# Kernel optimization log

Hardware: AMD Instinct MI355X
Metric: run time of the kernel (lower is better)

## Reference

```python
import jax, jax.numpy as jnp
import numpy as np

N = 16384

def _gcn_norm(edge_index, n):
    # PyG GCNConv: add self-loops, symmetric normalization D^-1/2 A_hat D^-1/2
    src = jnp.concatenate([edge_index[0], jnp.arange(n)])
    dst = jnp.concatenate([edge_index[1], jnp.arange(n)])
    deg = jax.ops.segment_sum(jnp.ones(src.shape[0], jnp.float32), dst, num_segments=n)
    dinv = jnp.where(deg > 0, jax.lax.rsqrt(deg), 0.0)
    w = dinv[src] * dinv[dst]  # [E + N]
    return src, dst, w

def _gcn_conv(x, W, b, src, dst, w, n):
    h = x @ W                                   # transform then propagate
    msg = w[:, None] * h[src]                   # gather + scale
    out = jax.ops.segment_sum(msg, dst, num_segments=n)  # scatter-add at targets
    return out + b

def setup_inputs() -> dict:
    key = jax.random.key(0)
    ks = jax.random.split(key, 8)
    E = 262144
    x = jax.random.normal(ks[0], (N, 128), jnp.float32)
    edge_index = jax.random.randint(ks[1], (2, E), 0, N, dtype=jnp.int64)
    W1 = jax.random.normal(ks[2], (128, 64), jnp.float32) * 0.1
    b1 = jnp.zeros((64,), jnp.float32)
    Wmu = jax.random.normal(ks[3], (64, 32), jnp.float32) * 0.1
    bmu = jnp.zeros((32,), jnp.float32)
    Wls = jax.random.normal(ks[4], (64, 32), jnp.float32) * 0.1
    bls = jnp.zeros((32,), jnp.float32)
    eps = jax.random.normal(ks[5], (N, 32), jnp.float32)
    return {"x": x, "edge_index": edge_index, "W1": W1, "b1": b1,
            "Wmu": Wmu, "bmu": bmu, "Wls": Wls, "bls": bls, "eps": eps}

def reference(x, edge_index, W1, b1, Wmu, bmu, Wls, bls, eps):
    n = x.shape[0]
    src, dst, w = _gcn_norm(edge_index, n)
    h = jax.nn.relu(_gcn_conv(x, W1, b1, src, dst, w, n))
    mu = _gcn_conv(h, Wmu, bmu, src, dst, w, n)
    logstd = _gcn_conv(h, Wls, bls, src, dst, w, n)
    z = mu + eps * jnp.exp(logstd)              # reparameterize
    adj_recon = jax.nn.sigmoid(z @ z.T)         # dense inner-product decode [N,N]
    return adj_recon, mu, logstd
```

## Files before the change

### kernel.cpp

```cpp
#include <hip/hip_runtime.h>

#define NN 16384
#define FIN 128
#define FH 64
#define FO 32

typedef __attribute__((ext_vector_type(8))) short bf16x8;
typedef __attribute__((ext_vector_type(4))) float f32x4;

__device__ inline unsigned short f2bf(float f) {
    unsigned int u = __float_as_uint(f);
    unsigned int r = (u + 0x7FFFu + ((u >> 16) & 1u)) >> 16;
    return (unsigned short)r;
}
__device__ inline float bf2f(unsigned short b) {
    return __uint_as_float((unsigned int)b << 16);
}


__global__ void k_zero(int* __restrict__ cnt) {
    int i = blockIdx.x * 256 + threadIdx.x;
    cnt[i] = 0;
}

__global__ void k_count(const int* __restrict__ dst, int* __restrict__ cnt, int E) {
    int e = blockIdx.x * 256 + threadIdx.x;
    if (e < E) atomicAdd(&cnt[dst[e] & (NN - 1)], 1);
}

__global__ __launch_bounds__(256) void k_scan(const int* __restrict__ cnt,
                                              int* __restrict__ row) {
    __shared__ int part[256];
    __shared__ int off[257];
    int t = threadIdx.x;
    int base = t * 64;
    int s = 0;
    for (int i = 0; i < 64; ++i) s += cnt[base + i];
    part[t] = s;
    __syncthreads();
    if (t == 0) {
        int a = 0;
        for (int i = 0; i < 256; ++i) { off[i] = a; a += part[i]; }
        off[256] = a;
    }
    __syncthreads();
    int a = off[t];
    for (int i = 0; i < 64; ++i) { row[base + i] = a; a += cnt[base + i]; }
    if (t == 0) row[NN] = off[256];
}

__global__ void k_dinv(const int* __restrict__ cnt, float* __restrict__ dinv,
                       int* __restrict__ cur) {
    int i = blockIdx.x * 256 + threadIdx.x;
    dinv[i] = rsqrtf((float)cnt[i] + 1.0f);
    cur[i] = 0;
}

__global__ void k_fill(const int* __restrict__ src, const int* __restrict__ dst,
                       const int* __restrict__ row, int* __restrict__ cur,
                       const float* __restrict__ dinv,
                       int* __restrict__ csr_s, float* __restrict__ csr_w, int E) {
    int e = blockIdx.x * 256 + threadIdx.x;
    if (e >= E) return;
    int s = src[e] & (NN - 1), d = dst[e] & (NN - 1);
    int pos = atomicAdd(&cur[d], 1);
    int slot = row[d] + pos;
    csr_s[slot] = s;
    csr_w[slot] = dinv[s] * dinv[d];
}


__global__ void k_h0(const float* __restrict__ x, const float* __restrict__ W1,
                     float* __restrict__ h0) {
    int row = blockIdx.x * 4 + (threadIdx.x >> 6);
    int col = threadIdx.x & 63;
    const float* xr = x + row * FIN;
    float acc = 0.f;
#pragma unroll 8
    for (int k = 0; k < FIN; ++k)
        acc = fmaf(xr[k], W1[k * FH + col], acc);
    h0[row * FH + col] = acc;
}

__global__ void k_t(const float* __restrict__ h, const float* __restrict__ Wmu,
                    const float* __restrict__ Wls, float* __restrict__ tmu,
                    float* __restrict__ tls) {
    int row = blockIdx.x * 4 + (threadIdx.x >> 6);
    int l = threadIdx.x & 63;
    const float* hr = h + row * FH;
    const float* W = (l < 32) ? Wmu : Wls;
    int c = l & 31;
    float acc = 0.f;
#pragma unroll 8
    for (int k = 0; k < FH; ++k)
        acc = fmaf(hr[k], W[k * FO + c], acc);
    if (l < 32) tmu[row * FO + c] = acc;
    else        tls[row * FO + c] = acc;
}


__global__ void k_prop1g(const int* __restrict__ row, const int* __restrict__ csr_s,
                         const float* __restrict__ csr_w, const float* __restrict__ dinv,
                         const float* __restrict__ h0, const float* __restrict__ b1,
                         float* __restrict__ h) {
    int t = blockIdx.x * 256 + threadIdx.x;
    int i = t >> 6, l = t & 63;
    int beg = row[i], end = row[i + 1];
    float di = dinv[i];
    float acc = di * di * h0[i * FH + l];
    for (int j = beg; j < end; ++j) {
        int s = csr_s[j];
        float w = csr_w[j];
        acc = fmaf(w, h0[s * FH + l], acc);
    }
    float v = acc + b1[l];
    h[i * FH + l] = v > 0.f ? v : 0.f;
}

__global__ void k_prop2g(const int* __restrict__ row, const int* __restrict__ csr_s,
                         const float* __restrict__ csr_w, const float* __restrict__ dinv,
                         const float* __restrict__ tmu, const float* __restrict__ tls,
                         const float* __restrict__ bmu, const float* __restrict__ bls,
                         const float* __restrict__ eps,
                         float* __restrict__ mu_out, float* __restrict__ ls_out,
                         unsigned short* __restrict__ zh, unsigned short* __restrict__ zl) {
    int t = blockIdx.x * 256 + threadIdx.x;
    int i = t >> 6, l = t & 63;
    int c = l & 31;
    int beg = row[i], end = row[i + 1];
    const float* tp = (l < 32) ? tmu : tls;
    float di = dinv[i];
    float acc = di * di * tp[i * FO + c];
    for (int j = beg; j < end; ++j) {
        int s = csr_s[j];
        float w = csr_w[j];
        acc = fmaf(w, tp[s * FO + c], acc);
    }
    float v = acc + ((l < 32) ? bmu[c] : bls[c]);
    if (l < 32) mu_out[i * FO + c] = v;
    else        ls_out[i * FO + c] = v;
    float other = __shfl_xor(v, 32);
    if (l < 32) {
        float zf = fmaf(eps[i * FO + c], __expf(other), v);
        unsigned short hb = f2bf(zf);
        zh[i * FO + c] = hb;
        zl[i * FO + c] = f2bf(zf - bf2f(hb));
    }
}

__global__ __launch_bounds__(256) void k_decode(const unsigned short* __restrict__ zh,
                                                const unsigned short* __restrict__ zl,
                                                float* __restrict__ out) {
    __shared__ float slab[4][16][264];
    int bj = blockIdx.x & 15, bi = blockIdx.x >> 4;
    int w = threadIdx.x >> 6;
    int l = threadIdx.x & 63;
    int lr = l & 15, lg = l >> 4;

    auto ld = [&](const unsigned short* p, int t) -> bf16x8 {
        return *(const bf16x8*)(p + ((size_t)t * 16 + lr) * FO + lg * 8);
    };

    bf16x8 rh = ld(zh, bi), rl = ld(zl, bi);

    int ctbase = bj * 64 + w * 16;
    bf16x8 ch[16], cl[16];
#pragma unroll
    for (int j = 0; j < 16; ++j) {
        ch[j] = ld(zh, ctbase + j);
        cl[j] = ld(zl, ctbase + j);
    }

#pragma unroll
    for (int j = 0; j < 16; ++j) {
        f32x4 a = {0.f, 0.f, 0.f, 0.f};
        a = __builtin_amdgcn_mfma_f32_16x16x32_bf16(ch[j], rh, a, 0, 0, 0);
        a = __builtin_amdgcn_mfma_f32_16x16x32_bf16(ch[j], rl, a, 0, 0, 0);
        a = __builtin_amdgcn_mfma_f32_16x16x32_bf16(cl[j], rh, a, 0, 0, 0);
        float4 v;
        v.x = __builtin_amdgcn_rcpf(1.f + __expf(-a[0]));
        v.y = __builtin_amdgcn_rcpf(1.f + __expf(-a[1]));
        v.z = __builtin_amdgcn_rcpf(1.f + __expf(-a[2]));
        v.w = __builtin_amdgcn_rcpf(1.f + __expf(-a[3]));
        *(float4*)&slab[w][lr][j * 16 + lg * 4] = v;
    }

#pragma unroll
    for (int r = 0; r < 16; ++r) {
        f32x4 v = *(const f32x4*)&slab[w][r][l * 4];
        f32x4* dst = (f32x4*)(out + ((size_t)(bi * 16 + r)) * NN
                              + bj * 1024 + w * 256 + l * 4);
        __builtin_nontemporal_store(v, dst);
    }
}


extern "C" void kernel_launch(void* const* d_in, const int* in_sizes, int n_in,
                              void* d_out, int out_size, void* d_ws, size_t ws_size,
                              hipStream_t stream) {
    const float* x    = (const float*)d_in[0];
    const int*   ei   = (const int*)d_in[1];
    const float* W1   = (const float*)d_in[2];
    const float* b1   = (const float*)d_in[3];
    const float* Wmu  = (const float*)d_in[4];
    const float* bmu  = (const float*)d_in[5];
    const float* Wls  = (const float*)d_in[6];
    const float* bls  = (const float*)d_in[7];
    const float* eps  = (const float*)d_in[8];

    int E = in_sizes[1] / 2;
    const int* src = ei;
    const int* dst = ei + E;

    float* ws = (float*)d_ws;
    float* dinv  = ws;
    int*   cnt   = (int*)(dinv + NN);
    int*   row   = cnt + NN;
    int*   cur   = row + NN + 16;
    int*   csr_s = cur + NN;
    float* csr_w = (float*)(csr_s + E);
    float* h0    = csr_w + E;
    float* h     = h0 + (size_t)NN * FH;
    float* tmu   = h  + (size_t)NN * FH;
    float* tls   = tmu + (size_t)NN * FO;
    unsigned short* zh = (unsigned short*)(tls + (size_t)NN * FO);
    unsigned short* zl = zh + (size_t)NN * FO;

    float* adj    = (float*)d_out;
    float* mu_out = adj + (size_t)NN * NN;
    float* ls_out = mu_out + (size_t)NN * FO;

    k_zero<<<NN / 256, 256, 0, stream>>>(cnt);
    k_count<<<(E + 255) / 256, 256, 0, stream>>>(dst, cnt, E);
    k_scan<<<1, 256, 0, stream>>>(cnt, row);
    k_dinv<<<NN / 256, 256, 0, stream>>>(cnt, dinv, cur);
    k_fill<<<(E + 255) / 256, 256, 0, stream>>>(src, dst, row, cur, dinv, csr_s, csr_w, E);
    k_h0<<<NN / 4, 256, 0, stream>>>(x, W1, h0);
    k_prop1g<<<NN * FH / 256, 256, 0, stream>>>(row, csr_s, csr_w, dinv, h0, b1, h);
    k_t<<<NN / 4, 256, 0, stream>>>(h, Wmu, Wls, tmu, tls);
    k_prop2g<<<NN * FH / 256, 256, 0, stream>>>(row, csr_s, csr_w, dinv, tmu, tls,
                                                bmu, bls, eps, mu_out, ls_out, zh, zl);
    k_decode<<<(NN / 16) * (NN / 1024), 256, 0, stream>>>(zh, zl, adj);
}
```

Before: 334.9 us.

## Fuse graph preprocessing kernels and restructure decode into two half-tile passes

Folds the dinv/cur initialisation into the scan kernel, merges CSR fill with the x@W1 transform into one launch, and fuses the first propagation with the second-layer weight transform using wave shuffles, removing the intermediate h buffer and several launches. The decode kernel now loads column tiles on the fly in two groups of eight, halving the LDS slab and requesting four blocks per CU for higher occupancy. The decode output is dominated by the 1 GiB adjacency write, so launch savings are small relative to total time, and the on-the-fly loads may expose more latency. There is also a leftover empty loop.

Measured after the change: 311.0 us. 7.1% less time.

```diff
diff --git a/kernel.cpp b/kernel.cpp
--- a/kernel.cpp
+++ b/kernel.cpp
@@ -29,7 +29,9 @@
 }
 
 __global__ __launch_bounds__(256) void k_scan(const int* __restrict__ cnt,
-                                              int* __restrict__ row) {
+                                              int* __restrict__ row,
+                                              float* __restrict__ dinv,
+                                              int* __restrict__ cur) {
     __shared__ int part[256];
     __shared__ int off[257];
     int t = threadIdx.x;
@@ -45,64 +47,47 @@
     }
     __syncthreads();
     int a = off[t];
-    for (int i = 0; i < 64; ++i) { row[base + i] = a; a += cnt[base + i]; }
+    for (int i = 0; i < 64; ++i) {
+        int c = cnt[base + i];
+        row[base + i] = a; a += c;
+        dinv[base + i] = rsqrtf((float)c + 1.0f);
+        cur[base + i] = 0;
+    }
     if (t == 0) row[NN] = off[256];
 }
 
-__global__ void k_dinv(const int* __restrict__ cnt, float* __restrict__ dinv,
-                       int* __restrict__ cur) {
-    int i = blockIdx.x * 256 + threadIdx.x;
-    dinv[i] = rsqrtf((float)cnt[i] + 1.0f);
-    cur[i] = 0;
-}
-
-__global__ void k_fill(const int* __restrict__ src, const int* __restrict__ dst,
-                       const int* __restrict__ row, int* __restrict__ cur,
-                       const float* __restrict__ dinv,
-                       int* __restrict__ csr_s, float* __restrict__ csr_w, int E) {
-    int e = blockIdx.x * 256 + threadIdx.x;
-    if (e >= E) return;
-    int s = src[e] & (NN - 1), d = dst[e] & (NN - 1);
-    int pos = atomicAdd(&cur[d], 1);
-    int slot = row[d] + pos;
-    csr_s[slot] = s;
-    csr_w[slot] = dinv[s] * dinv[d];
-}
-
-
-__global__ void k_h0(const float* __restrict__ x, const float* __restrict__ W1,
-                     float* __restrict__ h0) {
-    int row = blockIdx.x * 4 + (threadIdx.x >> 6);
-    int col = threadIdx.x & 63;
-    const float* xr = x + row * FIN;
-    float acc = 0.f;
+__global__ void k_fill_h0(const int* __restrict__ src, const int* __restrict__ dst,
+                          const int* __restrict__ row, int* __restrict__ cur,
+                          const float* __restrict__ dinv,
+                          int* __restrict__ csr_s, float* __restrict__ csr_w, int E, int nf,
+                          const float* __restrict__ x, const float* __restrict__ W1,
+                          float* __restrict__ h0) {
+    int b = blockIdx.x;
+    if (b < nf) {
+        int e = b * 256 + threadIdx.x;
+        if (e >= E) return;
+        int s = src[e] & (NN - 1), d = dst[e] & (NN - 1);
+        int pos = atomicAdd(&cur[d], 1);
+        int slot = row[d] + pos;
+        csr_s[slot] = s;
+        csr_w[slot] = dinv[s] * dinv[d];
+    } else {
+        int r = (b - nf) * 4 + (threadIdx.x >> 6);
+        int col = threadIdx.x & 63;
+        const float* xr = x + r * FIN;
+        float acc = 0.f;
 #pragma unroll 8
-    for (int k = 0; k < FIN; ++k)
-        acc = fmaf(xr[k], W1[k * FH + col], acc);
-    h0[row * FH + col] = acc;
-}
-
-__global__ void k_t(const float* __restrict__ h, const float* __restrict__ Wmu,
-                    const float* __restrict__ Wls, float* __restrict__ tmu,
-                    float* __restrict__ tls) {
-    int row = blockIdx.x * 4 + (threadIdx.x >> 6);
-    int l = threadIdx.x & 63;
-    const float* hr = h + row * FH;
-    const float* W = (l < 32) ? Wmu : Wls;
-    int c = l & 31;
-    float acc = 0.f;
-#pragma unroll 8
-    for (int k = 0; k < FH; ++k)
-        acc = fmaf(hr[k], W[k * FO + c], acc);
-    if (l < 32) tmu[row * FO + c] = acc;
-    else        tls[row * FO + c] = acc;
-}
-
-
-__global__ void k_prop1g(const int* __restrict__ row, const int* __restrict__ csr_s,
+        for (int k = 0; k < FIN; ++k)
+            acc = fmaf(xr[k], W1[k * FH + col], acc);
+        h0[r * FH + col] = acc;
+    }
+}
+
+__global__ void k_prop1t(const int* __restrict__ row, const int* __restrict__ csr_s,
                          const float* __restrict__ csr_w, const float* __restrict__ dinv,
                          const float* __restrict__ h0, const float* __restrict__ b1,
-                         float* __restrict__ h) {
+                         const float* __restrict__ Wmu, const float* __restrict__ Wls,
+                         float* __restrict__ tmu, float* __restrict__ tls) {
     int t = blockIdx.x * 256 + threadIdx.x;
     int i = t >> 6, l = t & 63;
     int beg = row[i], end = row[i + 1];
@@ -114,7 +99,16 @@
         acc = fmaf(w, h0[s * FH + l], acc);
     }
     float v = acc + b1[l];
-    h[i * FH + l] = v > 0.f ? v : 0.f;
+    v = v > 0.f ? v : 0.f;
+
+    const float* W = (l < 32) ? Wmu : Wls;
+    int c = l & 31;
+    float o = 0.f;
+#pragma unroll
+    for (int k = 0; k < FH; ++k)
+        o = fmaf(__shfl(v, k), W[k * FO + c], o);
+    if (l < 32) tmu[i * FO + c] = o;
+    else        tls[i * FO + c] = o;
 }
 
 __global__ void k_prop2g(const int* __restrict__ row, const int* __restrict__ csr_s,
@@ -148,10 +142,10 @@
     }
 }
 
-__global__ __launch_bounds__(256) void k_decode(const unsigned short* __restrict__ zh,
-                                                const unsigned short* __restrict__ zl,
-                                                float* __restrict__ out) {
-    __shared__ float slab[4][16][264];
+__global__ __launch_bounds__(256, 4) void k_decode(const unsigned short* __restrict__ zh,
+                                                   const unsigned short* __restrict__ zl,
+                                                   float* __restrict__ out) {
+    __shared__ float slab[4][16][136];
     int bj = blockIdx.x & 15, bi = blockIdx.x >> 4;
     int w = threadIdx.x >> 6;
     int l = threadIdx.x & 63;
@@ -164,33 +158,39 @@
     bf16x8 rh = ld(zh, bi), rl = ld(zl, bi);
 
     int ctbase = bj * 64 + w * 16;
-    bf16x8 ch[16], cl[16];
-#pragma unroll
-    for (int j = 0; j < 16; ++j) {
-        ch[j] = ld(zh, ctbase + j);
-        cl[j] = ld(zl, ctbase + j);
-    }
-
-#pragma unroll
-    for (int j = 0; j < 16; ++j) {
-        f32x4 a = {0.f, 0.f, 0.f, 0.f};
-        a = __builtin_amdgcn_mfma_f32_16x16x32_bf16(ch[j], rh, a, 0, 0, 0);
-        a = __builtin_amdgcn_mfma_f32_16x16x32_bf16(ch[j], rl, a, 0, 0, 0);
-        a = __builtin_amdgcn_mfma_f32_16x16x32_bf16(cl[j], rh, a, 0, 0, 0);
-        float4 v;
-        v.x = __builtin_amdgcn_rcpf(1.f + __expf(-a[0]));
-        v.y = __builtin_amdgcn_rcpf(1.f + __expf(-a[1]));
-        v.z = __builtin_amdgcn_rcpf(1.f + __expf(-a[2]));
-        v.w = __builtin_amdgcn_rcpf(1.f + __expf(-a[3]));
-        *(float4*)&slab[w][lr][j * 16 + lg * 4] = v;
-    }
-
-#pragma unroll
-    for (int r = 0; r < 16; ++r) {
-        f32x4 v = *(const f32x4*)&slab[w][r][l * 4];
-        f32x4* dst = (f32x4*)(out + ((size_t)(bi * 16 + r)) * NN
-                              + bj * 1024 + w * 256 + l * 4);
-        __builtin_nontemporal_store(v, dst);
+#pragma unroll
+    for (int g = 0; g < 2; ++g) {
+#pragma unroll
+        for (int j = 0; j < 8; ++j) {
+            int ct = ctbase + g * 8 + j;
+            bf16x8 ch = ld(zh, ct);
+            bf16x8 cl = ld(zl, ct);
+            f32x4 a = {0.f, 0.f, 0.f, 0.f};
+            a = __builtin_amdgcn_mfma_f32_16x16x32_bf16(ch, rh, a, 0, 0, 0);
+            a = __builtin_amdgcn_mfma_f32_16x16x32_bf16(ch, rl, a, 0, 0, 0);
+            a = __builtin_amdgcn_mfma_f32_16x16x32_bf16(cl, rh, a, 0, 0, 0);
+            float4 v;
+            v.x = __builtin_amdgcn_rcpf(1.f + __expf(-a[0]));
+            v.y = __builtin_amdgcn_rcpf(1.f + __expf(-a[1]));
+            v.z = __builtin_amdgcn_rcpf(1.f + __expf(-a[2]));
+            v.w = __builtin_amdgcn_rcpf(1.f + __expf(-a[3]));
+            *(float4*)&slab[w][lr][j * 16 + lg * 4] = v;
+        }
+        size_t cbase = (size_t)bj * 1024 + w * 256 + g * 128;
+#pragma unroll
+        for (int inst = 0; inst < 8; ++inst) {
+            int r = inst * 2 + (l >> 5);
+            int f4 = l & 31;
+            f32x4 v = *(const f32x4*)&slab[w][r][f4 * 4];
+            f32x4* dst = (f32x4*)(out + ((size_t)(bi * 16 + r)) * NN + cbase + f4 * 4);
+            __builtin_nontemporal_store(v, dst);
+        }
+#pragma unroll
+        for (int inst = 8; inst < 16; ++inst) {
+            int r = (inst - 8) * 2 + (l >> 5) + 0;
+            int r2 = inst * 2 - 16 + (l >> 5) + 0;
+            (void)r; (void)r2;
+        }
     }
 }
 
@@ -209,6 +209,7 @@
     const float* eps  = (const float*)d_in[8];
 
     int E = in_sizes[1] / 2;
+    int nf = (E + 255) / 256;
     const int* src = ei;
     const int* dst = ei + E;
 
@@ -220,8 +221,7 @@
     int*   csr_s = cur + NN;
     float* csr_w = (float*)(csr_s + E);
     float* h0    = csr_w + E;
-    float* h     = h0 + (size_t)NN * FH;
-    float* tmu   = h  + (size_t)NN * FH;
+    float* tmu   = h0 + (size_t)NN * FH;
     float* tls   = tmu + (size_t)NN * FO;
     unsigned short* zh = (unsigned short*)(tls + (size_t)NN * FO);
     unsigned short* zl = zh + (size_t)NN * FO;
@@ -231,13 +231,12 @@
     float* ls_out = mu_out + (size_t)NN * FO;
 
     k_zero<<<NN / 256, 256, 0, stream>>>(cnt);
-    k_count<<<(E + 255) / 256, 256, 0, stream>>>(dst, cnt, E);
-    k_scan<<<1, 256, 0, stream>>>(cnt, row);
-    k_dinv<<<NN / 256, 256, 0, stream>>>(cnt, dinv, cur);
-    k_fill<<<(E + 255) / 256, 256, 0, stream>>>(src, dst, row, cur, dinv, csr_s, csr_w, E);
-    k_h0<<<NN / 4, 256, 0, stream>>>(x, W1, h0);
-    k_prop1g<<<NN * FH / 256, 256, 0, stream>>>(row, csr_s, csr_w, dinv, h0, b1, h);
-    k_t<<<NN / 4, 256, 0, stream>>>(h, Wmu, Wls, tmu, tls);
+    k_count<<<nf, 256, 0, stream>>>(dst, cnt, E);
+    k_scan<<<1, 256, 0, stream>>>(cnt, row, dinv, cur);
+    k_fill_h0<<<nf + NN / 4, 256, 0, stream>>>(src, dst, row, cur, dinv,
+                                               csr_s, csr_w, E, nf, x, W1, h0);
+    k_prop1t<<<NN * FH / 256, 256, 0, stream>>>(row, csr_s, csr_w, dinv, h0, b1,
+                                                Wmu, Wls, tmu, tls);
     k_prop2g<<<NN * FH / 256, 256, 0, stream>>>(row, csr_s, csr_w, dinv, tmu, tls,
                                                 bmu, bls, eps, mu_out, ls_out, zh, zl);
     k_decode<<<(NN / 16) * (NN / 1024), 256, 0, stream>>>(zh, zl, adj);
```
